# Performance work log

Hardware: AMD Instinct MI355X
Metric: run time of the kernel (lower is better)

## Reference

```python
import jax, jax.numpy as jnp
import numpy as np

DIM = 128
NUM_HEADS = 2
WS = 8  # window_size


def setup_inputs() -> dict:
    key = jax.random.key(0)
    ks = jax.random.split(key, 8)
    B, C, H, W = 1, DIM, 64, 128  # W must equal DIM (proj acts on last spatial axis)
    w_scale = 1.0 / np.sqrt(DIM)
    return {
        "x": jax.random.normal(ks[0], (B, C, H, W), jnp.float32),
        "wavelet_features": jax.random.normal(ks[1], (B, C, H, W), jnp.float32),
        "Wq": jax.random.normal(ks[2], (DIM, DIM), jnp.float32) * w_scale,
        "bq": jnp.zeros((DIM,), jnp.float32),
        "Wk": jax.random.normal(ks[3], (DIM, DIM), jnp.float32) * w_scale,
        "bk": jnp.zeros((DIM,), jnp.float32),
        "Wv": jax.random.normal(ks[4], (DIM, DIM), jnp.float32) * w_scale,
        "bv": jnp.zeros((DIM,), jnp.float32),
        "Wp": jax.random.normal(ks[5], (DIM, DIM), jnp.float32) * w_scale,
        "bp": jnp.zeros((DIM,), jnp.float32),
    }


def _window_partition(t):
    # 'b c (h wh) (w ww) -> b (h w) (wh ww) c'
    B, C, H, W = t.shape
    h, w = H // WS, W // WS
    t = t.reshape(B, C, h, WS, w, WS)
    t = t.transpose(0, 2, 4, 3, 5, 1)  # B,h,w,wh,ww,C
    return t.reshape(B, h * w, WS * WS, C)


def reference(x, wavelet_features, Wq, bq, Wk, bk, Wv, bv, Wp, bp):
    B, C, H, W = x.shape
    hd = C // NUM_HEADS
    scale = hd ** (-0.5)

    xw = _window_partition(x)                   # [B, nW, ws*ws, C]
    ww = _window_partition(wavelet_features)    # [B, nW, ws*ws, C]

    q = xw @ Wq.T + bq
    k = ww @ Wk.T + bk
    v = ww @ Wv.T + bv

    # NOTE: original code flattens windows+tokens together, so attention is
    # GLOBAL over all N = H*W tokens (window partition is just a permutation).
    N = q.shape[1] * q.shape[2]
    q = q.reshape(B, N, NUM_HEADS, hd).transpose(0, 2, 1, 3)  # [B,h,N,d]
    k = k.reshape(B, N, NUM_HEADS, hd).transpose(0, 2, 1, 3)
    v = v.reshape(B, N, NUM_HEADS, hd).transpose(0, 2, 1, 3)

    attn = jax.nn.softmax(jnp.einsum('bhnd,bhmd->bhnm', q, k) * scale, axis=-1)
    out = jnp.einsum('bhnm,bhmd->bhnd', attn, v)  # [B,h,N,d]
    out = out.transpose(0, 2, 1, 3).reshape(B, N, C)

    # 'b (h w) (wh ww) c -> b c (h wh) (w ww)'
    h, w = H // WS, W // WS
    out = out.reshape(B, h, w, WS, WS, C).transpose(0, 5, 1, 3, 2, 4).reshape(B, C, H, W)

    # Faithful quirk: proj Linear acts on the LAST axis (spatial W == dim).
    out = out @ Wp.T + bp
    return out
```

## Files before the change

kernel.cpp:

```cpp
#include <hip/hip_runtime.h>
#include <stdint.h>

typedef float    f32x4  __attribute__((ext_vector_type(4)));
typedef __bf16   bf16x8 __attribute__((ext_vector_type(8)));
typedef short    s16x8  __attribute__((ext_vector_type(8)));
typedef int      i32x4  __attribute__((ext_vector_type(4)));
typedef unsigned short u16x4 __attribute__((ext_vector_type(4)));

#define DEVINL __device__ __forceinline__

DEVINL unsigned short f2bf(float f) {
  unsigned u = __builtin_bit_cast(unsigned, f);
  return (unsigned short)((u + 0x7fffu + ((u >> 16) & 1u)) >> 16);
}

DEVINL f32x4 mfma16(bf16x8 a, bf16x8 b, f32x4 c) {
  return __builtin_amdgcn_mfma_f32_16x16x32_bf16(a, b, c, 0, 0, 0);
}

DEVINL bf16x8 lds_frag(const unsigned char* p) {
  return __builtin_bit_cast(bf16x8, *(const s16x8*)p);
}

template <int CTRL>
DEVINL float dppf(float x) {
  int xi = __builtin_bit_cast(int, x);
  return __builtin_bit_cast(float, __builtin_amdgcn_update_dpp(xi, xi, CTRL, 0xF, 0xF, true));
}
DEVINL float redmax16(float v) {
  v = fmaxf(v, dppf<0xB1>(v));
  v = fmaxf(v, dppf<0x4E>(v));
  v = fmaxf(v, dppf<0x141>(v));
  v = fmaxf(v, dppf<0x140>(v));
  return v;
}

__global__ __launch_bounds__(256) void prep_w_kernel(
    const float* __restrict__ wq, const float* __restrict__ wk,
    const float* __restrict__ wv, const float* __restrict__ wp,
    unsigned short* __restrict__ wbf) {
  int id = blockIdx.x * 256 + threadIdx.x;
  int m = id >> 12;
  const float* src = (m == 0) ? wq : (m == 1) ? wk : (m == 2) ? wv : wp;
  f32x4 v = ((const f32x4*)src)[id & 4095];
  u16x4 o;
  o[0] = f2bf(v[0]); o[1] = f2bf(v[1]); o[2] = f2bf(v[2]); o[3] = f2bf(v[3]);
  ((u16x4*)wbf)[id] = o;
}

__global__ __launch_bounds__(256) void qkv_kernel(
    const float* __restrict__ x, const float* __restrict__ wav,
    const unsigned short* __restrict__ wbf,
    const float* __restrict__ bq, const float* __restrict__ bk, const float* __restrict__ bv,
    unsigned short* __restrict__ Qb, unsigned short* __restrict__ Kb,
    unsigned short* __restrict__ Vt) {
  __shared__ __align__(16) unsigned char sm[32768];
  const int tid = threadIdx.x;
  const int g = blockIdx.x >> 7;
  const int s0 = (blockIdx.x & 127) * 64;
  const float* srcm = (g == 0) ? x : wav;

  {
    const int c = tid >> 1, half = tid & 1;
    const float* xs = srcm + c * 8192 + s0 + half * 32;
#pragma unroll
    for (int i = 0; i < 8; ++i) {
      f32x4 vx = *(const f32x4*)(xs + i * 4);
#pragma unroll
      for (int j = 0; j < 4; ++j) {
        int s = half * 32 + i * 4 + j;
        int off = (c * 2) ^ ((s & 7) << 4);
        *(unsigned short*)(sm + s * 256 + off) = f2bf(vx[j]);
      }
    }
  }
  __syncthreads();

  const int w = tid >> 6, l = tid & 63, lr = l & 15, lh = l >> 4;
  const int arow = w * 16 + lr;
  const int aswz = (lr & 7) << 4;

  const unsigned char* asrc = sm + arow * 256;
  const unsigned char* wsrc = (const unsigned char*)wbf + g * 32768;
  f32x4 acc[8];
#pragma unroll
  for (int jt = 0; jt < 8; ++jt) acc[jt] = (f32x4){0.f, 0.f, 0.f, 0.f};
#pragma unroll
  for (int ks = 0; ks < 4; ++ks) {
    bf16x8 a = lds_frag(asrc + ((ks * 64 + lh * 16) ^ aswz));
#pragma unroll
    for (int jt = 0; jt < 8; ++jt) {
      bf16x8 bb = __builtin_bit_cast(
          bf16x8, *(const s16x8*)(wsrc + (jt * 16 + lr) * 256 + ks * 64 + lh * 16));
      acc[jt] = mfma16(a, bb, acc[jt]);
    }
  }
  if (g < 2) {
    const float* bias = g ? bk : bq;
    unsigned short* outp = g ? Kb : Qb;
#pragma unroll
    for (int jt = 0; jt < 8; ++jt) {
      float bb = bias[jt * 16 + lr];
#pragma unroll
      for (int r = 0; r < 4; ++r) {
        int row = s0 + w * 16 + lh * 4 + r;
        outp[row * 128 + jt * 16 + lr] = f2bf(acc[jt][r] + bb);
      }
    }
  } else {
    unsigned char* sm2 = sm + 16384;
#pragma unroll
    for (int jt = 0; jt < 8; ++jt) {
      float bb = bv[jt * 16 + lr];
#pragma unroll
      for (int r = 0; r < 4; ++r) {
        int jj = jt * 16 + lr;
        int sl = w * 16 + lh * 4 + r;
        *(unsigned short*)(sm2 + jj * 128 + ((sl * 2) ^ ((jj & 7) << 4))) =
            f2bf(acc[jt][r] + bb);
      }
    }
    __syncthreads();
#pragma unroll
    for (int g2 = 0; g2 < 4; ++g2) {
      int jj = w * 32 + g2 * 8 + (l >> 3);
      s16x8 row = *(const s16x8*)(sm2 + jj * 128 + (((l & 7) * 16) ^ ((jj & 7) << 4)));
      *(s16x8*)(Vt + jj * 8192 + s0 + (l & 7) * 8) = row;
    }
  }
}

__global__ __launch_bounds__(256) void attn_kernel(
    const unsigned short* __restrict__ Qb, const unsigned short* __restrict__ Kb,
    const unsigned short* __restrict__ Vt, float* __restrict__ Opart,
    float* __restrict__ Ml, float* __restrict__ Ll, int NIT) {
  __shared__ __align__(16) unsigned char sm[32768];
  const int tid = threadIdx.x;
  const int bid = blockIdx.x;
  const int hq = bid & 255, sp = bid >> 8;
  const int h = hq & 1, q0 = (hq >> 1) * 64;
  const int t0 = sp * NIT;
  const int w = tid >> 6, l = tid & 63, lr = l & 15, lh = l >> 4;
  const int lswz = (lr & 7) << 4;

  bf16x8 qf[2];
#pragma unroll
  for (int ks = 0; ks < 2; ++ks)
    qf[ks] = __builtin_bit_cast(
        bf16x8, *(const s16x8*)(Qb + (q0 + w * 16 + lr) * 128 + h * 64 + ks * 32 + lh * 8));

  const s16x8 ones_i = {0x3F80, 0x3F80, 0x3F80, 0x3F80, 0x3F80, 0x3F80, 0x3F80, 0x3F80};
  const bf16x8 onesf = __builtin_bit_cast(bf16x8, ones_i);

  f32x4 acc[4];
  float m_[4], l_[4];
#pragma unroll
  for (int i = 0; i < 4; ++i) { acc[i] = (f32x4){0.f,0.f,0.f,0.f}; m_[i] = -1e30f; l_[i] = 0.f; }

  int kglob[4], kldsoff[4], vglob[4], vldsoff[4];
#pragma unroll
  for (int i = 0; i < 4; ++i) {
    int ch = tid + i * 256;
    int key = ch >> 3, slot = ch & 7;
    int kr = key & 63;
    kldsoff[i] = (key >> 6) * 8192 + kr * 128 + ((slot * 16) ^ ((kr & 7) << 4));
    kglob[i] = key * 128 + h * 64 + slot * 8;
    int d = ch >> 4, kslot = ch & 15;
    vldsoff[i] = 16384 + (kslot >> 3) * 8192 + d * 128 +
                 (((kslot & 7) * 16) ^ ((d & 7) << 4));
    vglob[i] = (h * 64 + d) * 8192 + kslot * 8;
  }

  {
#pragma unroll
    for (int i = 0; i < 4; ++i) {
      i32x4 kv = *(const i32x4*)(Kb + (size_t)t0 * 16384 + kglob[i]);
      i32x4 vv = *(const i32x4*)(Vt + (size_t)t0 * 128 + vglob[i]);
      *(i32x4*)(sm + kldsoff[i]) = kv;
      *(i32x4*)(sm + vldsoff[i]) = vv;
    }
  }
  __syncthreads();

  const float sc = 0.18033688011112042f;

  for (int tt = 0; tt < NIT; ++tt) {
    i32x4 nk[4], nv[4];
    if (tt < NIT - 1) {
#pragma unroll
      for (int i = 0; i < 4; ++i) {
        nk[i] = *(const i32x4*)(Kb + (size_t)(t0 + tt + 1) * 16384 + kglob[i]);
        nv[i] = *(const i32x4*)(Vt + (size_t)(t0 + tt + 1) * 128 + vglob[i]);
      }
    }

    f32x4 s8[8];
#pragma unroll
    for (int nt = 0; nt < 8; ++nt) s8[nt] = (f32x4){0.f,0.f,0.f,0.f};
#pragma unroll
    for (int ks = 0; ks < 2; ++ks) {
#pragma unroll
      for (int nt = 0; nt < 8; ++nt) {
        const unsigned char* kf_p = sm + (nt >> 2) * 8192 + ((nt & 3) * 16 + lr) * 128 +
                                    ((ks * 64 + lh * 16) ^ lswz);
        s8[nt] = mfma16(qf[ks], lds_frag(kf_p), s8[nt]);
      }
    }

#pragma unroll
    for (int r = 0; r < 4; ++r) {
      float mx = s8[0][r];
#pragma unroll
      for (int nt = 1; nt < 8; ++nt) mx = fmaxf(mx, s8[nt][r]);
      mx = redmax16(mx) * sc;
      float mn = fmaxf(m_[r], mx);
      float al = __builtin_amdgcn_exp2f(m_[r] - mn);
      m_[r] = mn;
      l_[r] *= al;
#pragma unroll
      for (int nt = 0; nt < 8; ++nt)
        s8[nt][r] = __builtin_amdgcn_exp2f(fmaf(s8[nt][r], sc, -mn));
#pragma unroll
      for (int ct = 0; ct < 4; ++ct) acc[ct][r] *= al;
    }

    __syncthreads();

    const int qrow = w * 16 + lh * 4;
#pragma unroll
    for (int r = 0; r < 4; r += 2) {
      int qa = qrow + r, qb2 = qrow + r + 1;
      int swza = (qa & 7) << 4, swzb = (qb2 & 7) << 4;
#pragma unroll
      for (int nt = 0; nt < 8; ++nt) {
        unsigned u;
        asm("v_cvt_pk_bf16_f32 %0, %1, %2" : "=v"(u) : "v"(s8[nt][r]), "v"(s8[nt][r + 1]));
        unsigned char* pan = sm + (nt >> 2) * 8192;
        int koff = (nt & 3) * 32 + lr * 2;
        *(unsigned short*)(pan + qa * 128 + (koff ^ swza)) = (unsigned short)u;
        *(unsigned short*)(pan + qb2 * 128 + (koff ^ swzb)) = (unsigned short)(u >> 16);
      }
    }
    asm volatile("s_waitcnt lgkmcnt(0)" ::: "memory");
    __builtin_amdgcn_sched_barrier(0);

    bf16x8 pa[4];
#pragma unroll
    for (int ks = 0; ks < 4; ++ks)
      pa[ks] = lds_frag(sm + (ks >> 1) * 8192 + (w * 16 + lr) * 128 +
                        (((ks & 1) * 64 + lh * 16) ^ lswz));
    f32x4 lt4 = (f32x4){0.f,0.f,0.f,0.f};
#pragma unroll
    for (int ks = 0; ks < 4; ++ks) {
      lt4 = mfma16(pa[ks], onesf, lt4);
      const unsigned char* vpan = sm + 16384 + (ks >> 1) * 8192;
#pragma unroll
      for (int ct = 0; ct < 4; ++ct) {
        bf16x8 vf = lds_frag(vpan + (ct * 16 + lr) * 128 +
                             (((ks & 1) * 64 + lh * 16) ^ lswz));
        acc[ct] = mfma16(pa[ks], vf, acc[ct]);
      }
    }
#pragma unroll
    for (int r = 0; r < 4; ++r) l_[r] += lt4[r];

    __syncthreads();
    if (tt < NIT - 1) {
#pragma unroll
      for (int i = 0; i < 4; ++i) {
        *(i32x4*)(sm + kldsoff[i]) = nk[i];
        *(i32x4*)(sm + vldsoff[i]) = nv[i];
      }
    }
    __syncthreads();
  }

  float* op = Opart + (size_t)bid * 4096;
#pragma unroll
  for (int ct = 0; ct < 4; ++ct) {
#pragma unroll
    for (int r = 0; r < 4; ++r) {
      int q = w * 16 + lh * 4 + r;
      op[q * 64 + ct * 16 + lr] = acc[ct][r];
    }
  }
  if (lr == 0) {
#pragma unroll
    for (int r = 0; r < 4; ++r) {
      int q = w * 16 + lh * 4 + r;
      Ml[bid * 64 + q] = m_[r];
      Ll[bid * 64 + q] = l_[r];
    }
  }
}

__global__ __launch_bounds__(256) void combine_kernel(
    const float* __restrict__ Opart, const float* __restrict__ Ml,
    const float* __restrict__ Ll, unsigned short* __restrict__ Ot, int S) {
  __shared__ float wgt_s[8][32];
  __shared__ float rinv_s[32];
  __shared__ unsigned short lt[64][34];
  const int bid = blockIdx.x;
  const int hq = bid >> 1, half = bid & 1;
  const int h = hq & 1, q0 = (hq >> 1) * 64;
  const int t = threadIdx.x;

  if (t < 32) {
    int qg = half * 32 + t;
    float m8[8];
    float M = -1e30f;
    for (int sp = 0; sp < S; ++sp) {
      m8[sp] = Ml[(size_t)(sp * 256 + hq) * 64 + qg];
      M = fmaxf(M, m8[sp]);
    }
    float L = 0.f;
    for (int sp = 0; sp < S; ++sp) {
      float wv = __builtin_amdgcn_exp2f(m8[sp] - M);
      wgt_s[sp][t] = wv;
      L += Ll[(size_t)(sp * 256 + hq) * 64 + qg] * wv;
    }
    rinv_s[t] = 1.0f / L;
  }
  __syncthreads();

  const int q = t >> 3;
  const int dc = t & 7;
  const int qg = half * 32 + q;
  f32x4 o0 = (f32x4){0.f,0.f,0.f,0.f}, o1 = (f32x4){0.f,0.f,0.f,0.f};
  for (int sp = 0; sp < S; ++sp) {
    const f32x4* src =
        (const f32x4*)(Opart + (size_t)(sp * 256 + hq) * 4096 + qg * 64 + dc * 8);
    float wv = wgt_s[sp][q];
    o0 += src[0] * wv;
    o1 += src[1] * wv;
  }
  float rinv = rinv_s[q];
#pragma unroll
  for (int j = 0; j < 4; ++j) lt[dc * 8 + j][q] = f2bf(o0[j] * rinv);
#pragma unroll
  for (int j = 0; j < 4; ++j) lt[dc * 8 + 4 + j][q] = f2bf(o1[j] * rinv);
  __syncthreads();

  const int d = t >> 2, q8 = (t & 3) * 8;
  unsigned short tmp[8];
#pragma unroll
  for (int j = 0; j < 8; ++j) tmp[j] = lt[d][q8 + j];
  *(s16x8*)(Ot + (size_t)(h * 64 + d) * 8192 + q0 + half * 32 + q8) = *(s16x8*)tmp;
}

__global__ __launch_bounds__(256) void proj_kernel(
    const unsigned short* __restrict__ Ot, const unsigned short* __restrict__ wbf,
    const float* __restrict__ bp, float* __restrict__ out) {
  __shared__ __align__(16) unsigned char sm[16384];
  const int tid = threadIdx.x;
  const int r0 = blockIdx.x * 64;
#pragma unroll
  for (int i = 0; i < 4; ++i) {
    int chk = tid + 256 * i;
    i32x4 v = *(const i32x4*)(Ot + r0 * 128 + chk * 8);
    int row = chk >> 4, off = (chk & 15) * 16;
    *(i32x4*)(sm + row * 256 + (off ^ ((row & 7) << 4))) = v;
  }
  __syncthreads();
  const int w = tid >> 6, l = tid & 63, lr = l & 15, lh = l >> 4;
  f32x4 acc[8];
#pragma unroll
  for (int jt = 0; jt < 8; ++jt) acc[jt] = (f32x4){0.f, 0.f, 0.f, 0.f};
  const unsigned char* wsrc = (const unsigned char*)wbf + 3 * 32768;
#pragma unroll
  for (int ks = 0; ks < 4; ++ks) {
    bf16x8 a = lds_frag(sm + (w * 16 + lr) * 256 + ((ks * 64 + lh * 16) ^ ((lr & 7) << 4)));
#pragma unroll
    for (int jt = 0; jt < 8; ++jt) {
      bf16x8 bb = __builtin_bit_cast(
          bf16x8, *(const s16x8*)(wsrc + (jt * 16 + lr) * 256 + ks * 64 + lh * 16));
      acc[jt] = mfma16(a, bb, acc[jt]);
    }
  }
#pragma unroll
  for (int jt = 0; jt < 8; ++jt) {
    float bb = bp[jt * 16 + lr];
#pragma unroll
    for (int r = 0; r < 4; ++r)
      out[(r0 + w * 16 + lh * 4 + r) * 128 + jt * 16 + lr] = acc[jt][r] + bb;
  }
}

extern "C" void kernel_launch(void* const* d_in, const int* in_sizes, int n_in,
                              void* d_out, int out_size, void* d_ws, size_t ws_size,
                              hipStream_t stream) {
  const float* x   = (const float*)d_in[0];
  const float* wav = (const float*)d_in[1];
  const float* Wq  = (const float*)d_in[2];
  const float* bq  = (const float*)d_in[3];
  const float* Wk  = (const float*)d_in[4];
  const float* bk  = (const float*)d_in[5];
  const float* Wv  = (const float*)d_in[6];
  const float* bv  = (const float*)d_in[7];
  const float* Wp  = (const float*)d_in[8];
  const float* bp  = (const float*)d_in[9];
  (void)in_sizes; (void)n_in; (void)out_size;

  unsigned char* ws = (unsigned char*)d_ws;
  unsigned short* Qb  = (unsigned short*)(ws);
  unsigned short* Kb  = (unsigned short*)(ws + 2097152);
  unsigned short* Vt  = (unsigned short*)(ws + 4194304);
  unsigned short* Ot  = (unsigned short*)(ws + 6291456);
  unsigned short* Wbf = (unsigned short*)(ws + 8388608);

  const size_t pbase = 8519680;
  int S = 8;
  while (S > 1 && pbase + (size_t)S * 4325376 > ws_size) S >>= 1;
  float* Opart = (float*)(ws + pbase);
  float* Ml    = (float*)(ws + pbase + (size_t)S * 4194304);
  float* Ll    = (float*)(ws + pbase + (size_t)S * 4194304 + (size_t)S * 65536);
  const int NIT = 64 / S;

  prep_w_kernel<<<64, 256, 0, stream>>>(Wq, Wk, Wv, Wp, Wbf);
  qkv_kernel<<<384, 256, 0, stream>>>(x, wav, Wbf, bq, bk, bv, Qb, Kb, Vt);
  attn_kernel<<<256 * S, 256, 0, stream>>>(Qb, Kb, Vt, Opart, Ml, Ll, NIT);
  combine_kernel<<<512, 256, 0, stream>>>(Opart, Ml, Ll, Ot, S);
  proj_kernel<<<128, 256, 0, stream>>>(Ot, Wbf, bp, (float*)d_out);
}
```

Baseline: 122.0 us.

## Load K and V MFMA fragments directly from global memory instead of LDS

The attention kernel no longer stages K and V tiles through shared memory with register prefetch and block barriers. Each wave now reads its K and V MFMA fragments straight from global memory (relying on cache), LDS shrinks to hold only the P tile, and two syncthreads per iteration are dropped. Because all four waves read the same K/V data, this multiplies global/L2 traffic by four and exposes load latency with no software prefetch. The P tile is still written and read per wave in LDS without a barrier, which looks safe only because each wave touches only its own rows.

```diff
diff --git a/kernel.cpp b/kernel.cpp
--- a/kernel.cpp
+++ b/kernel.cpp
@@ -19,6 +19,9 @@
 }
 
 DEVINL bf16x8 lds_frag(const unsigned char* p) {
+  return __builtin_bit_cast(bf16x8, *(const s16x8*)p);
+}
+DEVINL bf16x8 gmem_frag(const unsigned short* p) {
   return __builtin_bit_cast(bf16x8, *(const s16x8*)p);
 }
 
@@ -134,7 +137,7 @@
     const unsigned short* __restrict__ Qb, const unsigned short* __restrict__ Kb,
     const unsigned short* __restrict__ Vt, float* __restrict__ Opart,
     float* __restrict__ Ml, float* __restrict__ Ll, int NIT) {
-  __shared__ __align__(16) unsigned char sm[32768];
+  __shared__ __align__(16) unsigned char sm[16384];
   const int tid = threadIdx.x;
   const int bid = blockIdx.x;
   const int hq = bid & 255, sp = bid >> 8;
@@ -157,42 +160,14 @@
 #pragma unroll
   for (int i = 0; i < 4; ++i) { acc[i] = (f32x4){0.f,0.f,0.f,0.f}; m_[i] = -1e30f; l_[i] = 0.f; }
 
-  int kglob[4], kldsoff[4], vglob[4], vldsoff[4];
-#pragma unroll
-  for (int i = 0; i < 4; ++i) {
-    int ch = tid + i * 256;
-    int key = ch >> 3, slot = ch & 7;
-    int kr = key & 63;
-    kldsoff[i] = (key >> 6) * 8192 + kr * 128 + ((slot * 16) ^ ((kr & 7) << 4));
-    kglob[i] = key * 128 + h * 64 + slot * 8;
-    int d = ch >> 4, kslot = ch & 15;
-    vldsoff[i] = 16384 + (kslot >> 3) * 8192 + d * 128 +
-                 (((kslot & 7) * 16) ^ ((d & 7) << 4));
-    vglob[i] = (h * 64 + d) * 8192 + kslot * 8;
-  }
-
-  {
-#pragma unroll
-    for (int i = 0; i < 4; ++i) {
-      i32x4 kv = *(const i32x4*)(Kb + (size_t)t0 * 16384 + kglob[i]);
-      i32x4 vv = *(const i32x4*)(Vt + (size_t)t0 * 128 + vglob[i]);
-      *(i32x4*)(sm + kldsoff[i]) = kv;
-      *(i32x4*)(sm + vldsoff[i]) = vv;
-    }
-  }
-  __syncthreads();
-
   const float sc = 0.18033688011112042f;
 
+  const unsigned short* kbase = Kb + (size_t)lr * 128 + h * 64 + lh * 8;
+  const unsigned short* vbase = Vt + (size_t)(h * 64 + lr) * 8192 + lh * 8;
+
   for (int tt = 0; tt < NIT; ++tt) {
-    i32x4 nk[4], nv[4];
-    if (tt < NIT - 1) {
-#pragma unroll
-      for (int i = 0; i < 4; ++i) {
-        nk[i] = *(const i32x4*)(Kb + (size_t)(t0 + tt + 1) * 16384 + kglob[i]);
-        nv[i] = *(const i32x4*)(Vt + (size_t)(t0 + tt + 1) * 128 + vglob[i]);
-      }
-    }
+    const size_t kT = (size_t)(t0 + tt) * 128 * 128;
+    const size_t vT = (size_t)(t0 + tt) * 128;
 
     f32x4 s8[8];
 #pragma unroll
@@ -201,9 +176,9 @@
     for (int ks = 0; ks < 2; ++ks) {
 #pragma unroll
       for (int nt = 0; nt < 8; ++nt) {
-        const unsigned char* kf_p = sm + (nt >> 2) * 8192 + ((nt & 3) * 16 + lr) * 128 +
-                                    ((ks * 64 + lh * 16) ^ lswz);
-        s8[nt] = mfma16(qf[ks], lds_frag(kf_p), s8[nt]);
+        bf16x8 kf = gmem_frag(kbase + kT + (size_t)((nt >> 2) * 64 + (nt & 3) * 16) * 128 +
+                              ks * 32);
+        s8[nt] = mfma16(qf[ks], kf, s8[nt]);
       }
     }
 
@@ -224,21 +199,19 @@
       for (int ct = 0; ct < 4; ++ct) acc[ct][r] *= al;
     }
 
-    __syncthreads();
-
     const int qrow = w * 16 + lh * 4;
 #pragma unroll
     for (int r = 0; r < 4; r += 2) {
-      int qa = qrow + r, qb2 = qrow + r + 1;
-      int swza = (qa & 7) << 4, swzb = (qb2 & 7) << 4;
+      int qa = qrow + r, qb = qrow + r + 1;
+      int swza = (qa & 7) << 4, swzb = (qb & 7) << 4;
 #pragma unroll
       for (int nt = 0; nt < 8; ++nt) {
+        int pbase = (nt >> 2) * 8192;
+        int koff = (nt & 3) * 32 + lr * 2;
         unsigned u;
         asm("v_cvt_pk_bf16_f32 %0, %1, %2" : "=v"(u) : "v"(s8[nt][r]), "v"(s8[nt][r + 1]));
-        unsigned char* pan = sm + (nt >> 2) * 8192;
-        int koff = (nt & 3) * 32 + lr * 2;
-        *(unsigned short*)(pan + qa * 128 + (koff ^ swza)) = (unsigned short)u;
-        *(unsigned short*)(pan + qb2 * 128 + (koff ^ swzb)) = (unsigned short)(u >> 16);
+        *(unsigned short*)(sm + pbase + qa * 128 + (koff ^ swza)) = (unsigned short)u;
+        *(unsigned short*)(sm + pbase + qb * 128 + (koff ^ swzb)) = (unsigned short)(u >> 16);
       }
     }
     asm volatile("s_waitcnt lgkmcnt(0)" ::: "memory");
@@ -253,26 +226,15 @@
 #pragma unroll
     for (int ks = 0; ks < 4; ++ks) {
       lt4 = mfma16(pa[ks], onesf, lt4);
-      const unsigned char* vpan = sm + 16384 + (ks >> 1) * 8192;
+      size_t vko = vT + (ks >> 1) * 64 + (ks & 1) * 32;
 #pragma unroll
       for (int ct = 0; ct < 4; ++ct) {
-        bf16x8 vf = lds_frag(vpan + (ct * 16 + lr) * 128 +
-                             (((ks & 1) * 64 + lh * 16) ^ lswz));
+        bf16x8 vf = gmem_frag(vbase + (size_t)(ct * 16) * 8192 + vko);
         acc[ct] = mfma16(pa[ks], vf, acc[ct]);
       }
     }
 #pragma unroll
     for (int r = 0; r < 4; ++r) l_[r] += lt4[r];
-
-    __syncthreads();
-    if (tt < NIT - 1) {
-#pragma unroll
-      for (int i = 0; i < 4; ++i) {
-        *(i32x4*)(sm + kldsoff[i]) = nk[i];
-        *(i32x4*)(sm + vldsoff[i]) = nv[i];
-      }
-    }
-    __syncthreads();
   }
 
   float* op = Opart + (size_t)bid * 4096;
```

After: 270.4 us. +121.7%, slower.
